# Kernel optimization log

Hardware: AMD Instinct MI355X
Metric: run time of the kernel (lower is better)

The kernel has to match this reference:

```python
import jax, jax.numpy as jnp
import numpy as np

DIM = 768
NUM_SS = 8
INNER = DIM // 4  # s_ratio = 4 -> 192


def setup_inputs() -> dict:
    key = jax.random.key(0)
    ks = jax.random.split(key, 9)
    s = 0.02
    return {
        "x": jax.random.normal(ks[0], (16, 4096, DIM), dtype=jnp.float32),
        "Wq": jax.random.normal(ks[1], (DIM, DIM), dtype=jnp.float32) * s,
        "bq": jax.random.normal(ks[2], (DIM,), dtype=jnp.float32) * s,
        "Wk": jax.random.normal(ks[3], (DIM, NUM_SS * INNER), dtype=jnp.float32) * s,
        "bk": jax.random.normal(ks[4], (NUM_SS * INNER,), dtype=jnp.float32) * s,
        "Wv": jax.random.normal(ks[5], (DIM, DIM), dtype=jnp.float32) * s,
        "bv": jax.random.normal(ks[6], (DIM,), dtype=jnp.float32) * s,
        "Wss_out": jax.random.normal(ks[7], (INNER, DIM), dtype=jnp.float32) * s,
        "bss_out": jax.random.normal(ks[8], (DIM,), dtype=jnp.float32) * s,
    }


def reference(x, Wq, bq, Wk, bk, Wv, bv, Wss_out, bss_out):
    b = x.shape[0]
    ss_tokens = x[:, -NUM_SS:, :]          # [b, S, D]
    reg = x[:, :-NUM_SS, :]                # [b, T, D]
    x_v = reg @ Wv + bv                    # [b, T, D]
    x_q = reg @ Wq + bq                    # [b, T, D]
    x_k = reg @ Wk + bk                    # [b, T, S*I]
    # mean over regular tokens, reshape to one inner vector per ss token
    ss_update_ = jnp.mean(x_k, axis=1).reshape(b, NUM_SS, INNER)
    new_ss = ss_tokens + (ss_update_ @ Wss_out + bss_out)     # [b, S, D]
    scale = jnp.asarray(1.0 / np.sqrt(DIM), x.dtype)
    sim = jnp.einsum('btd,bsd->bts', x_q, new_ss) * scale     # [b, T, S]
    attn = jax.nn.softmax(sim, axis=-1)
    upd = jnp.einsum('bts,bsd->btd', attn, new_ss)            # [b, T, D]
    new_reg = jax.nn.relu(x_v + upd)
    return jnp.concatenate([new_reg, new_ss], axis=1)
```

## Files before the change

kernel.cpp:

```cpp
#include <hip/hip_runtime.h>
#include <hip/hip_bf16.h>

#define B_ 16
#define T_ 4096
#define TREG 4088
#define D_ 768
#define NSS 8
#define INNER_ 192
#define NK 1536
#define NCHUNK 128

typedef unsigned int u32;
typedef unsigned short u16;
typedef __attribute__((ext_vector_type(8))) short bf16x8;
typedef __attribute__((ext_vector_type(4))) float f32x4;

__device__ __forceinline__ u16 f2bf(float f) {
  union { __hip_bfloat16 h; u16 u; } cv;
  cv.h = __float2bfloat16(f);
  return cv.u;
}

__device__ __forceinline__ void load16_lds(const void* g, void* l) {
  __builtin_amdgcn_global_load_lds(
      (const __attribute__((address_space(1))) u32*)(unsigned long long)g,
      (__attribute__((address_space(3))) u32*)(u32)(unsigned long long)l,
      16, 0, 0);
}

__global__ __launch_bounds__(256) void k_wvt(const float* __restrict__ Wv,
                                             u16* __restrict__ wvT) {
  __shared__ float tile[16][17];
  int tx = threadIdx.x & 15, ty = threadIdx.x >> 4;
  int nb = blockIdx.x * 16, kb = blockIdx.y * 16;
  tile[ty][tx] = Wv[(size_t)(kb + ty) * D_ + nb + tx];
  __syncthreads();
  wvT[(size_t)(nb + ty) * D_ + kb + tx] = f2bf(tile[tx][ty]);
}

template <bool CONV>
__global__ __launch_bounds__(192) void k_conv_mean(const float* __restrict__ x,
                                                   u16* __restrict__ xb,
                                                   float* __restrict__ partials) {
  int b = blockIdx.y, tc = blockIdx.x, tid = threadIdx.x;
  const float4* xp = (const float4*)(x + (size_t)(b * T_ + tc * 32) * D_) + tid;
  ushort4* op = nullptr;
  if (CONV) op = ((ushort4*)(xb + (size_t)(b * T_ + tc * 32) * D_)) + tid;
  float s0 = 0, s1 = 0, s2 = 0, s3 = 0;
  int tbase = tc * 32;
#pragma unroll 4
  for (int tt = 0; tt < 32; ++tt) {
    float4 v = xp[(size_t)tt * 192];
    if (CONV) {
      ushort4 o;
      o.x = f2bf(v.x); o.y = f2bf(v.y); o.z = f2bf(v.z); o.w = f2bf(v.w);
      op[(size_t)tt * 192] = o;
    }
    if (tbase + tt < TREG) { s0 += v.x; s1 += v.y; s2 += v.z; s3 += v.w; }
  }
  float4 st; st.x = s0; st.y = s1; st.z = s2; st.w = s3;
  ((float4*)(partials + ((size_t)b * NCHUNK + tc) * D_))[tid] = st;
}

__global__ __launch_bounds__(256) void k_ssu(const float* __restrict__ partials,
                                             const float* __restrict__ Wk,
                                             const float* __restrict__ bk,
                                             float* __restrict__ ssu) {
  int b = blockIdx.y, tid = threadIdx.x;
  int n = blockIdx.x * 256 + tid;
  __shared__ float mv[D_];
  for (int d = tid; d < D_; d += 256) {
    const float* p = partials + (size_t)b * NCHUNK * D_ + d;
    float s = 0;
#pragma unroll 8
    for (int c = 0; c < NCHUNK; ++c) s += p[(size_t)c * D_];
    mv[d] = s * (1.0f / TREG);
  }
  __syncthreads();
  float a = bk[n];
#pragma unroll 8
  for (int d = 0; d < D_; ++d) a += mv[d] * Wk[(size_t)d * NK + n];
  ssu[(size_t)b * NK + n] = a;
}

__global__ __launch_bounds__(256) void k_nss(
    const float* __restrict__ x, const float* __restrict__ ssu,
    const float* __restrict__ Wss, const float* __restrict__ bss,
    const float* __restrict__ bq, float* __restrict__ out,
    float* __restrict__ nssf, u16* __restrict__ nssT, float* __restrict__ qb) {
  int s = blockIdx.x, b = blockIdx.y, tid = threadIdx.x;
  __shared__ float su[INNER_];
  __shared__ float qred[4];
  if (tid < INNER_) su[tid] = ssu[(size_t)b * NK + s * INNER_ + tid];
  __syncthreads();
  size_t xr = (size_t)(b * T_ + TREG + s) * D_;
  float a0 = x[xr + tid]       + bss[tid];
  float a1 = x[xr + tid + 256] + bss[tid + 256];
  float a2 = x[xr + tid + 512] + bss[tid + 512];
#pragma unroll 4
  for (int i = 0; i < INNER_; ++i) {
    float sv = su[i];
    const float* wr = Wss + (size_t)i * D_ + tid;
    a0 += sv * wr[0]; a1 += sv * wr[256]; a2 += sv * wr[512];
  }
  out[xr + tid] = a0; out[xr + tid + 256] = a1; out[xr + tid + 512] = a2;
  size_t nb = (size_t)(b * NSS + s) * D_;
  nssf[nb + tid] = a0; nssf[nb + tid + 256] = a1; nssf[nb + tid + 512] = a2;
  size_t tb = (size_t)b * D_;
  nssT[(tb + tid) * NSS + s] = f2bf(a0);
  nssT[(tb + tid + 256) * NSS + s] = f2bf(a1);
  nssT[(tb + tid + 512) * NSS + s] = f2bf(a2);
  float q = bq[tid] * a0 + bq[tid + 256] * a1 + bq[tid + 512] * a2;
#pragma unroll
  for (int o = 1; o < 64; o <<= 1) q += __shfl_xor(q, o, 64);
  if ((tid & 63) == 0) qred[tid >> 6] = q;
  __syncthreads();
  if (tid == 0) qb[b * NSS + s] = qred[0] + qred[1] + qred[2] + qred[3];
}

__global__ __launch_bounds__(256) void k_wqs(const float* __restrict__ Wq,
                                             const float* __restrict__ nssf,
                                             u16* __restrict__ wqsT) {
  __shared__ float nss[NSS * (D_ + 4)];
  int b = blockIdx.y, tid = threadIdx.x;
  int o = blockIdx.x * 256 + tid;
  int j = o >> 3, s = o & 7;
  for (int i = tid; i < NSS * D_; i += 256) {
    int s2 = i / D_, d2 = i - s2 * D_;
    nss[s2 * (D_ + 4) + d2] = nssf[(size_t)b * NSS * D_ + i];
  }
  __syncthreads();
  const float* wr = Wq + (size_t)j * D_;
  const float* nr = nss + s * (D_ + 4);
  float a = 0;
#pragma unroll 8
  for (int d = 0; d < D_; ++d) a += wr[d] * nr[d];
  wqsT[((size_t)b * NSS + s) * D_ + j] = f2bf(a);
}

template <bool ABF16>
__global__ __launch_bounds__(256, 3) void k_main(
    const u16* __restrict__ xb, const float* __restrict__ xf,
    const u16* __restrict__ wvT, const u16* __restrict__ wqsT,
    const u16* __restrict__ nssTg, const float* __restrict__ qb,
    const float* __restrict__ bv, float* __restrict__ out) {
  __shared__ uint4 ldsv[2112];
  u16* lds = (u16*)ldsv;
  u16* As0 = lds;
  u16* Bs0 = lds + 4096;
  u16* As1 = lds + 8448;
  u16* Bs1 = lds + 12544;

  const int tid = threadIdx.x;
  const int g = blockIdx.x;
  const int xcd = g & 7;
  const int li = g >> 3;
  const int nblk = li % 6;
  const int pair = li / 6;
  const int pid = pair * 8 + xcd;
  const int t0 = (pid & 31) * 128;
  const int b = pid >> 5;
  const int n0 = nblk * 128;

  const int wave = tid >> 6, lane = tid & 63;
  const int wy = wave >> 1, wx = wave & 1;
  const int lr = lane & 15, lq = lane >> 4;

  const int ar = tid >> 2;
  const int agc = (tid & 3) ^ ((ar >> 1) & 3);
  const int fch = (lq ^ ((lr >> 1) & 3)) * 8;

  const u16* Bg = wvT + (size_t)n0 * D_;
  const u16* Qg = wqsT + (size_t)b * NSS * D_;
  const int qs = tid >> 2;
  const int qgc = (tid & 3) ^ ((qs >> 1) & 3);

  const u16* Ag16 = ABF16 ? (xb + (size_t)(b * T_ + t0) * D_) : nullptr;
  const float* Agf = ABF16 ? nullptr : (xf + (size_t)(b * T_ + t0) * D_);

  f32x4 acc[4][4];
  f32x4 sacc[4];
#pragma unroll
  for (int i = 0; i < 4; ++i) {
    sacc[i] = f32x4{0.f, 0.f, 0.f, 0.f};
#pragma unroll
    for (int j = 0; j < 4; ++j) acc[i][j] = f32x4{0.f, 0.f, 0.f, 0.f};
  }

  auto STAGE = [&](u16* As, u16* Bs, int k0) {
    if constexpr (ABF16) {
      load16_lds(Ag16 + (size_t)ar * D_ + k0 + agc * 8, As + tid * 8);
      load16_lds(Ag16 + (size_t)(ar + 64) * D_ + k0 + agc * 8,
                 As + (tid + 256) * 8);
    } else {
      const float* p0 = Agf + (size_t)ar * D_ + k0 + agc * 8;
      const float* p1 = Agf + (size_t)(ar + 64) * D_ + k0 + agc * 8;
      float4 a0 = *(const float4*)p0, a1 = *(const float4*)(p0 + 4);
      float4 a2 = *(const float4*)p1, a3 = *(const float4*)(p1 + 4);
      ushort4 w0, w1, w2, w3;
      w0.x = f2bf(a0.x); w0.y = f2bf(a0.y); w0.z = f2bf(a0.z); w0.w = f2bf(a0.w);
      w1.x = f2bf(a1.x); w1.y = f2bf(a1.y); w1.z = f2bf(a1.z); w1.w = f2bf(a1.w);
      w2.x = f2bf(a2.x); w2.y = f2bf(a2.y); w2.z = f2bf(a2.z); w2.w = f2bf(a2.w);
      w3.x = f2bf(a3.x); w3.y = f2bf(a3.y); w3.z = f2bf(a3.z); w3.w = f2bf(a3.w);
      *(ushort4*)(As + tid * 8) = w0; *(ushort4*)(As + tid * 8 + 4) = w1;
      *(ushort4*)(As + (tid + 256) * 8) = w2;
      *(ushort4*)(As + (tid + 256) * 8 + 4) = w3;
    }
    load16_lds(Bg + (size_t)ar * D_ + k0 + agc * 8, Bs + tid * 8);
    load16_lds(Bg + (size_t)(ar + 64) * D_ + k0 + agc * 8, Bs + (tid + 256) * 8);
    if (tid < 32)
      load16_lds(Qg + (size_t)qs * D_ + k0 + qgc * 8, Bs + 4096 + tid * 8);
  };

  auto COMPUTE = [&](const u16* As, const u16* Bs) {
    bf16x8 af[4], bfr[4], qf;
#pragma unroll
    for (int mt = 0; mt < 4; ++mt)
      af[mt] = *(const bf16x8*)(As + (wy * 64 + mt * 16 + lr) * 32 + fch);
#pragma unroll
    for (int nt = 0; nt < 4; ++nt)
      bfr[nt] = *(const bf16x8*)(Bs + (wx * 64 + nt * 16 + lr) * 32 + fch);
    qf = *(const bf16x8*)(Bs + (128 + (lr & 7)) * 32 + fch);
#pragma unroll
    for (int mt = 0; mt < 4; ++mt) {
#pragma unroll
      for (int nt = 0; nt < 4; ++nt)
        acc[mt][nt] = __builtin_amdgcn_mfma_f32_16x16x32_bf16(
            af[mt], bfr[nt], acc[mt][nt], 0, 0, 0);
      sacc[mt] = __builtin_amdgcn_mfma_f32_16x16x32_bf16(
          af[mt], qf, sacc[mt], 0, 0, 0);
    }
  };

  STAGE(As0, Bs0, 0);
  __syncthreads();
#pragma unroll 1
  for (int k0 = 0; k0 < D_; k0 += 64) {
    STAGE(As1, Bs1, k0 + 32);
    COMPUTE(As0, Bs0);
    __syncthreads();
    if (k0 + 64 < D_) STAGE(As0, Bs0, k0 + 64);
    COMPUTE(As1, Bs1);
    __syncthreads();
  }

  u16* anb = lds;
  u16* nsl = lds + 4096;
  {
    uint4 z; z.x = z.y = z.z = z.w = 0;
    if (tid < 128) {
      uint4 v = *(const uint4*)(nssTg + ((size_t)b * D_ + n0 + tid) * NSS);
      int sw = ((tid >> 1) & 3) * 8;
      *(uint4*)(nsl + tid * 32 + sw) = v;
      *(uint4*)(nsl + tid * 32 + (sw ^ 8)) = z;
      *(uint4*)(nsl + tid * 32 + (sw ^ 16)) = z;
      *(uint4*)(nsl + tid * 32 + (sw ^ 24)) = z;
    } else {
      int r = tid - 128;
      *(uint4*)(anb + r * 32) = z;
      *(uint4*)(anb + r * 32 + 8) = z;
      *(uint4*)(anb + r * 32 + 16) = z;
      *(uint4*)(anb + r * 32 + 24) = z;
    }
  }
  __syncthreads();

  const float scale = 0.03608439182435161f;
  const float qbias = (lr < 8) ? qb[b * NSS + lr] : 0.f;
#pragma unroll
  for (int mt = 0; mt < 4; ++mt) {
    f32x4 s4 = sacc[mt];
#pragma unroll
    for (int r = 0; r < 4; ++r) {
      float v = (lr < 8) ? (s4[r] + qbias) * scale : -1.0e30f;
      float mx = v;
      mx = fmaxf(mx, __shfl_xor(mx, 1, 16));
      mx = fmaxf(mx, __shfl_xor(mx, 2, 16));
      mx = fmaxf(mx, __shfl_xor(mx, 4, 16));
      float e = (lr < 8) ? __expf(v - mx) : 0.f;
      float sm = e;
      sm += __shfl_xor(sm, 1, 16);
      sm += __shfl_xor(sm, 2, 16);
      sm += __shfl_xor(sm, 4, 16);
      if (lr < 8) {
        float a = e / sm;
        int row = wy * 64 + mt * 16 + lq * 4 + r;
        anb[row * 32 + ((row >> 1) & 3) * 8 + lr] = f2bf(a);
      }
    }
  }
  __syncthreads();

  bf16x8 nf[4];
#pragma unroll
  for (int nt = 0; nt < 4; ++nt)
    nf[nt] = *(const bf16x8*)(nsl + (wx * 64 + nt * 16 + lr) * 32 + fch);
#pragma unroll
  for (int mt = 0; mt < 4; ++mt) {
    bf16x8 afr =
        *(const bf16x8*)(anb + (wy * 64 + mt * 16 + lr) * 32 + fch);
#pragma unroll
    for (int nt = 0; nt < 4; ++nt)
      acc[mt][nt] = __builtin_amdgcn_mfma_f32_16x16x32_bf16(
          afr, nf[nt], acc[mt][nt], 0, 0, 0);
  }

  float bvv[4];
#pragma unroll
  for (int nt = 0; nt < 4; ++nt) bvv[nt] = bv[n0 + wx * 64 + nt * 16 + lr];
#pragma unroll
  for (int mt = 0; mt < 4; ++mt) {
    int trow = wy * 64 + mt * 16 + lq * 4;
#pragma unroll
    for (int r = 0; r < 4; ++r) {
      int token = t0 + trow + r;
      if (token < TREG) {
        float* op = out + ((size_t)b * T_ + token) * D_ + n0 + wx * 64;
#pragma unroll
        for (int nt = 0; nt < 4; ++nt)
          op[nt * 16 + lr] = fmaxf(acc[mt][nt][r] + bvv[nt], 0.f);
      }
    }
  }
}

extern "C" void kernel_launch(void* const* d_in, const int* in_sizes, int n_in,
                              void* d_out, int out_size, void* d_ws, size_t ws_size,
                              hipStream_t stream) {
  (void)in_sizes; (void)n_in; (void)out_size;
  const float* x   = (const float*)d_in[0];
  const float* Wq  = (const float*)d_in[1];
  const float* bq  = (const float*)d_in[2];
  const float* Wk  = (const float*)d_in[3];
  const float* bk  = (const float*)d_in[4];
  const float* Wv  = (const float*)d_in[5];
  const float* bv  = (const float*)d_in[6];
  const float* Wss = (const float*)d_in[7];
  const float* bss = (const float*)d_in[8];
  float* out = (float*)d_out;

  const size_t SZ_XB   = (size_t)B_ * T_ * D_ * 2;
  const size_t SZ_WVT  = (size_t)D_ * D_ * 2;
  const size_t SZ_PART = (size_t)B_ * NCHUNK * D_ * 4;
  const size_t SZ_SSU  = (size_t)B_ * NK * 4;
  const size_t SZ_NSSF = (size_t)B_ * NSS * D_ * 4;
  const size_t SZ_NSST = (size_t)B_ * D_ * NSS * 2;
  const size_t SZ_QB   = (size_t)B_ * NSS * 4;
  const size_t SZ_WQS  = (size_t)B_ * NSS * D_ * 2;
  const size_t SMALL = SZ_WVT + SZ_PART + SZ_SSU + SZ_NSSF + SZ_NSST + SZ_QB + SZ_WQS;
  const size_t FULL = SZ_XB + SMALL;
  const bool big = ws_size >= FULL;

  char* ws = (char*)d_ws;
  size_t off = big ? SZ_XB : 0;
  u16*   xb    = (u16*)ws;
  u16*   wvT   = (u16*)(ws + off);   off += SZ_WVT;
  float* parts = (float*)(ws + off); off += SZ_PART;
  float* ssu   = (float*)(ws + off); off += SZ_SSU;
  float* nssf  = (float*)(ws + off); off += SZ_NSSF;
  u16*   nssT  = (u16*)(ws + off);   off += SZ_NSST;
  float* qbb   = (float*)(ws + off); off += SZ_QB;
  u16*   wqsT  = (u16*)(ws + off);   off += SZ_WQS;

  k_wvt<<<dim3(48, 48), 256, 0, stream>>>(Wv, wvT);
  if (big)
    k_conv_mean<true><<<dim3(NCHUNK, 16), 192, 0, stream>>>(x, xb, parts);
  else
    k_conv_mean<false><<<dim3(NCHUNK, 16), 192, 0, stream>>>(x, nullptr, parts);
  k_ssu<<<dim3(6, 16), 256, 0, stream>>>(parts, Wk, bk, ssu);
  k_nss<<<dim3(NSS, 16), 256, 0, stream>>>(x, ssu, Wss, bss, bq, out, nssf, nssT, qbb);
  k_wqs<<<dim3(24, 16), 256, 0, stream>>>(Wq, nssf, wqsT);
  if (big)
    k_main<true><<<3072, 256, 0, stream>>>(xb, x, wvT, wqsT, nssT, qbb, bv, out);
  else
    k_main<false><<<3072, 256, 0, stream>>>(nullptr, x, wvT, wqsT, nssT, qbb, bv, out);
}
```

Measured before the change: 601.9 us.

## Triple-buffer LDS staging with vmcnt-based waits in bf16 main GEMM loop

For the bf16-input path, the main GEMM loop now uses three LDS stages instead of two, issuing global-to-LDS loads two k-steps ahead. A full __syncthreads is replaced by an explicit s_waitcnt vmcnt(5) plus s_barrier, so newer loads can stay in flight while older stages are consumed. The Q-row load is redistributed so every wave issues the same number of loads, which keeps per-wave vmcnt counts uniform. LDS use grows by half, which may reduce occupancy under launch_bounds(256,3).

```diff
diff --git a/kernel.cpp b/kernel.cpp
--- a/kernel.cpp
+++ b/kernel.cpp
@@ -144,12 +144,11 @@
     const u16* __restrict__ wvT, const u16* __restrict__ wqsT,
     const u16* __restrict__ nssTg, const float* __restrict__ qb,
     const float* __restrict__ bv, float* __restrict__ out) {
-  __shared__ uint4 ldsv[2112];
+  __shared__ uint4 ldsv[3168];
   u16* lds = (u16*)ldsv;
-  u16* As0 = lds;
-  u16* Bs0 = lds + 4096;
-  u16* As1 = lds + 8448;
-  u16* Bs1 = lds + 12544;
+  u16* As0 = lds;          u16* Bs0 = lds + 4096;
+  u16* As1 = lds + 8448;   u16* Bs1 = lds + 12544;
+  u16* As2 = lds + 16896;  u16* Bs2 = lds + 20992;
 
   const int tid = threadIdx.x;
   const int g = blockIdx.x;
@@ -172,8 +171,8 @@
 
   const u16* Bg = wvT + (size_t)n0 * D_;
   const u16* Qg = wqsT + (size_t)b * NSS * D_;
-  const int qs = tid >> 2;
-  const int qgc = (tid & 3) ^ ((qs >> 1) & 3);
+  const int qrow = 2 * wave + ((lane >> 2) & 1);
+  const int qc = (lane & 3) ^ wave;
 
   const u16* Ag16 = ABF16 ? (xb + (size_t)(b * T_ + t0) * D_) : nullptr;
   const float* Agf = ABF16 ? nullptr : (xf + (size_t)(b * T_ + t0) * D_);
@@ -208,8 +207,9 @@
     }
     load16_lds(Bg + (size_t)ar * D_ + k0 + agc * 8, Bs + tid * 8);
     load16_lds(Bg + (size_t)(ar + 64) * D_ + k0 + agc * 8, Bs + (tid + 256) * 8);
-    if (tid < 32)
-      load16_lds(Qg + (size_t)qs * D_ + k0 + qgc * 8, Bs + 4096 + tid * 8);
+    if (lane < 8)
+      load16_lds(Qg + (size_t)qrow * D_ + k0 + qc * 8,
+                 Bs + 4096 + wave * 64 + lane * 8);
   };
 
   auto COMPUTE = [&](const u16* As, const u16* Bs) {
@@ -232,16 +232,42 @@
     }
   };
 
-  STAGE(As0, Bs0, 0);
-  __syncthreads();
+  auto WAIT5 = [&]() {
+    asm volatile("s_waitcnt vmcnt(5) lgkmcnt(0)" ::: "memory");
+    __builtin_amdgcn_s_barrier();
+    __builtin_amdgcn_sched_barrier(0);
+  };
+  auto WAIT0 = [&]() {
+    asm volatile("s_waitcnt vmcnt(0) lgkmcnt(0)" ::: "memory");
+    __builtin_amdgcn_s_barrier();
+    __builtin_amdgcn_sched_barrier(0);
+  };
+
+  if constexpr (ABF16) {
+    STAGE(As0, Bs0, 0);
+    STAGE(As1, Bs1, 32);
+    int kk = 0;
 #pragma unroll 1
-  for (int k0 = 0; k0 < D_; k0 += 64) {
-    STAGE(As1, Bs1, k0 + 32);
-    COMPUTE(As0, Bs0);
+    for (int it = 0; it < 7; ++it, kk += 96) {
+      WAIT5(); STAGE(As2, Bs2, kk + 64);  COMPUTE(As0, Bs0);
+      WAIT5(); STAGE(As0, Bs0, kk + 96);  COMPUTE(As1, Bs1);
+      WAIT5(); STAGE(As1, Bs1, kk + 128); COMPUTE(As2, Bs2);
+    }
+    WAIT5(); STAGE(As2, Bs2, 736); COMPUTE(As0, Bs0);
+    WAIT5(); COMPUTE(As1, Bs1);
+    WAIT0(); COMPUTE(As2, Bs2);
+  } else {
+    STAGE(As0, Bs0, 0);
     __syncthreads();
-    if (k0 + 64 < D_) STAGE(As0, Bs0, k0 + 64);
-    COMPUTE(As1, Bs1);
-    __syncthreads();
+#pragma unroll 1
+    for (int k0 = 0; k0 < D_; k0 += 64) {
+      STAGE(As1, Bs1, k0 + 32);
+      COMPUTE(As0, Bs0);
+      __syncthreads();
+      if (k0 + 64 < D_) STAGE(As0, Bs0, k0 + 64);
+      COMPUTE(As1, Bs1);
+      __syncthreads();
+    }
   }
 
   u16* anb = lds;
```

Measured after the change: 598.0 us. Within noise of the previous version (-0.7%).
